# Performance work log

Measured on AMD Instinct MI355X. Metric: run time of the kernel, lower is better.

## Reference

```python
import jax, jax.numpy as jnp
import numpy as np

N = 50000
E = 400000
IN_FEATS = 256
HIDDEN = 64
HEADS = 8
CLASSES = 40
NEG_SLOPE = 0.2  # DGL GATConv default negative_slope


def setup_inputs() -> dict:
    key = jax.random.key(0)
    ks = jax.random.split(key, 12)
    features = jax.random.normal(ks[0], (N, IN_FEATS), dtype=jnp.float32)
    src = jax.random.randint(ks[1], (E,), 0, N, dtype=jnp.int32)
    dst = jax.random.randint(ks[2], (E,), 0, N, dtype=jnp.int32)
    s = 0.05
    # layer 0: in_feats -> HEADS*HIDDEN
    W1 = jax.random.normal(ks[3], (IN_FEATS, HEADS * HIDDEN), dtype=jnp.float32) * s
    al1 = jax.random.normal(ks[4], (HEADS, HIDDEN), dtype=jnp.float32) * s
    ar1 = jax.random.normal(ks[5], (HEADS, HIDDEN), dtype=jnp.float32) * s
    # layer 1: HEADS*HIDDEN -> HEADS*HIDDEN
    W2 = jax.random.normal(ks[6], (HEADS * HIDDEN, HEADS * HIDDEN), dtype=jnp.float32) * s
    al2 = jax.random.normal(ks[7], (HEADS, HIDDEN), dtype=jnp.float32) * s
    ar2 = jax.random.normal(ks[8], (HEADS, HIDDEN), dtype=jnp.float32) * s
    # layer 2: HEADS*HIDDEN -> 1*CLASSES
    W3 = jax.random.normal(ks[9], (HEADS * HIDDEN, CLASSES), dtype=jnp.float32) * s
    al3 = jax.random.normal(ks[10], (1, CLASSES), dtype=jnp.float32) * s
    ar3 = jax.random.normal(ks[11], (1, CLASSES), dtype=jnp.float32) * s
    return {"features": features, "src": src, "dst": dst,
            "W1": W1, "al1": al1, "ar1": ar1,
            "W2": W2, "al2": al2, "ar2": ar2,
            "W3": W3, "al3": al3, "ar3": ar3}


def gat_conv(h, W, al, ar, src, dst):
    """DGL GATConv (no bias, no residual, no activation, no dropout)."""
    H, D = al.shape
    feat = (h @ W).reshape(N, H, D)                      # [N,H,D]
    el = jnp.sum(feat * al[None], axis=-1)               # [N,H]
    er = jnp.sum(feat * ar[None], axis=-1)               # [N,H]
    e = jax.nn.leaky_relu(el[src] + er[dst], NEG_SLOPE)  # [E,H]
    # edge softmax over incoming edges of each dst node
    m = jax.ops.segment_max(e, dst, num_segments=N)      # [N,H]
    ex = jnp.exp(e - m[dst])                             # [E,H]
    denom = jax.ops.segment_sum(ex, dst, num_segments=N) # [N,H]
    alpha = ex / denom[dst]                              # [E,H]
    msg = alpha[:, :, None] * feat[src]                  # [E,H,D]
    out = jax.ops.segment_sum(msg, dst, num_segments=N)  # [N,H,D]
    return out.reshape(N, H * D)


def reference(features, src, dst, W1, al1, ar1, W2, al2, ar2, W3, al3, ar3):
    h = gat_conv(features, W1, al1, ar1, src, dst)  # [N, HEADS*HIDDEN]
    h = gat_conv(h, W2, al2, ar2, src, dst)         # [N, HEADS*HIDDEN]
    h = gat_conv(h, W3, al3, ar3, src, dst)         # [N, CLASSES]
    return h
```

## Files before the change

### kernel.cpp

```cpp
#include <hip/hip_runtime.h>
#include <hip/hip_bf16.h>

#define NN 50000
#define NE 400000
#define MPAD 50048

typedef __bf16 bf16x8_t __attribute__((ext_vector_type(8)));
typedef float f32x4_t __attribute__((ext_vector_type(4)));

__device__ __forceinline__ float bhi(unsigned int u) {
    union { unsigned int i; float f; } v; v.i = u & 0xffff0000u; return v.f;
}
__device__ __forceinline__ float blo(unsigned int u) {
    union { unsigned int i; float f; } v; v.i = u << 16; return v.f;
}

__global__ __launch_bounds__(256) void prep_kernel(
    const float* __restrict__ features, __hip_bfloat16* __restrict__ Abf,
    const int* __restrict__ dst, int* __restrict__ deg,
    const float* __restrict__ W1, __hip_bfloat16* __restrict__ W1t,
    const float* __restrict__ W2, __hip_bfloat16* __restrict__ W2t,
    const float* __restrict__ W3, __hip_bfloat16* __restrict__ W3t,
    const float* __restrict__ al1, const float* __restrict__ ar1,
    const float* __restrict__ al2, const float* __restrict__ ar2,
    __hip_bfloat16* __restrict__ walr1, __hip_bfloat16* __restrict__ walr2) {
    int stride = gridDim.x * blockDim.x;
    for (int i = blockIdx.x * blockDim.x + threadIdx.x; i < NN * 256; i += stride) {
        Abf[i] = __float2bfloat16(features[i]);
        if (i < NE) atomicAdd(&deg[dst[i]], 1);
        if (i < 512 * 256) {
            int n = i >> 8, k = i & 255;
            W1t[i] = __float2bfloat16(W1[k * 512 + n]);
        }
        if (i < 512 * 512) {
            int n = i >> 9, k = i & 511;
            W2t[i] = __float2bfloat16(W2[k * 512 + n]);
        }
        if (i < 48 * 512) {
            int n = i >> 9, k = i & 511;
            W3t[i] = __float2bfloat16((n < 40) ? W3[k * 40 + n] : 0.f);
        }
        if (i < 16 * 256) {
            int j = i >> 8, k = i & 255;
            const float* v = (j < 8) ? (al1 + j * 64) : (ar1 + (j - 8) * 64);
            float s = 0.f;
            for (int d = 0; d < 64; ++d) s += W1[(size_t)k * 512 + (j & 7) * 64 + d] * v[d];
            walr1[(k >> 5) * 512 + j * 32 + (k & 31)] = __float2bfloat16(s);
        }
        if (i < 16 * 512) {
            int j = i >> 9, k = i & 511;
            const float* v = (j < 8) ? (al2 + j * 64) : (ar2 + (j - 8) * 64);
            float s = 0.f;
            for (int d = 0; d < 64; ++d) s += W2[(size_t)k * 512 + (j & 7) * 64 + d] * v[d];
            walr2[(k >> 5) * 512 + j * 32 + (k & 31)] = __float2bfloat16(s);
        }
    }
}

__global__ void scan_kernel(const int* __restrict__ deg, int* __restrict__ off,
                            int* __restrict__ cur, int n) {
    __shared__ int wsum[16];
    __shared__ int carry_s;
    const int tid = threadIdx.x;
    const int lane = tid & 63, wid = tid >> 6;
    if (tid == 0) carry_s = 0;
    __syncthreads();
    for (int base = 0; base < n; base += 1024) {
        int i = base + tid;
        int v = (i < n) ? deg[i] : 0;
        int s = v;
        for (int o = 1; o < 64; o <<= 1) {
            int t = __shfl_up(s, o, 64);
            if (lane >= o) s += t;
        }
        if (lane == 63) wsum[wid] = s;
        __syncthreads();
        if (wid == 0) {
            int ws = (lane < 16) ? wsum[lane] : 0;
            for (int o = 1; o < 16; o <<= 1) {
                int t = __shfl_up(ws, o, 64);
                if (lane >= o) ws += t;
            }
            if (lane < 16) wsum[lane] = ws;
        }
        __syncthreads();
        int wpre = (wid == 0) ? 0 : wsum[wid - 1];
        int carry = carry_s;
        int excl = carry + wpre + s - v;
        if (i < n) { off[i] = excl; cur[i] = excl; }
        __syncthreads();
        if (tid == 1023) carry_s = carry + wsum[15];
    }
    __syncthreads();
    if (tid == 0) off[n] = carry_s;
}

__global__ void scatter_kernel(const int* __restrict__ src, const int* __restrict__ dst,
                               int* __restrict__ cur, int* __restrict__ csr_src) {
    int e = blockIdx.x * blockDim.x + threadIdx.x;
    if (e < NE) {
        int p = atomicAdd(&cur[dst[e]], 1);
        csr_src[p] = src[e];
    }
}

__device__ __forceinline__ void gld_lds16(const void* g, void* l) {
    __builtin_amdgcn_global_load_lds(
        (const __attribute__((address_space(1))) unsigned int*)g,
        (__attribute__((address_space(3))) unsigned int*)l, 16, 0, 0);
}

__global__ __launch_bounds__(256) void gemm_bt_fused(const __hip_bfloat16* __restrict__ A,
                                                     const __hip_bfloat16* __restrict__ Wt,
                                                     const __hip_bfloat16* __restrict__ walr,
                                                     __hip_bfloat16* __restrict__ C,
                                                     float* __restrict__ el,
                                                     float* __restrict__ er,
                                                     int K) {
    __shared__ __align__(16) char smem[16384];
    char* smemA = smem;
    char* smemB = smem + 8192;
    const int w = threadIdx.x >> 6;
    const int lane = threadIdx.x & 63;
    const int row0 = blockIdx.x * 128;
    const int col0 = blockIdx.y * 128;
    const int quad = lane >> 4, l15 = lane & 15;
    const int wm = (w >> 1) * 64, wn = (w & 1) * 64;
    const int c0 = w * 2;
    const int srow = lane >> 2;
    const int skel = (lane & 3) * 8;
    const bool my_e = (blockIdx.y == 0) && ((w & 1) == 0);

    f32x4_t acc[4][4] = {};
    f32x4_t acce[4] = {};
    for (int k0 = 0; k0 < K; k0 += 32) {
        __syncthreads();
        {
            const __hip_bfloat16* gA0 = A + (size_t)(row0 + c0 * 16 + srow) * K + k0 + skel;
            const __hip_bfloat16* gB0 = Wt + (size_t)(col0 + c0 * 16 + srow) * K + k0 + skel;
            gld_lds16(gA0, smemA + c0 * 1024);
            gld_lds16(gA0 + (size_t)16 * K, smemA + (c0 + 1) * 1024);
            gld_lds16(gB0, smemB + c0 * 1024);
            gld_lds16(gB0 + (size_t)16 * K, smemB + (c0 + 1) * 1024);
        }
        __syncthreads();
        bf16x8_t a[4], b[4];
#pragma unroll
        for (int mi = 0; mi < 4; mi++)
            a[mi] = *reinterpret_cast<const bf16x8_t*>(smemA + (wm + mi * 16 + l15) * 64 + quad * 16);
#pragma unroll
        for (int ni = 0; ni < 4; ni++)
            b[ni] = *reinterpret_cast<const bf16x8_t*>(smemB + (wn + ni * 16 + l15) * 64 + quad * 16);
#pragma unroll
        for (int mi = 0; mi < 4; mi++)
#pragma unroll
            for (int ni = 0; ni < 4; ni++)
                acc[mi][ni] = __builtin_amdgcn_mfma_f32_16x16x32_bf16(a[mi], b[ni], acc[mi][ni], 0, 0, 0);
        if (my_e) {
            bf16x8_t b5 = *reinterpret_cast<const bf16x8_t*>(
                walr + (k0 >> 5) * 512 + l15 * 32 + quad * 8);
#pragma unroll
            for (int mi = 0; mi < 4; mi++)
                acce[mi] = __builtin_amdgcn_mfma_f32_16x16x32_bf16(a[mi], b5, acce[mi], 0, 0, 0);
        }
    }
#pragma unroll
    for (int mi = 0; mi < 4; mi++) {
#pragma unroll
        for (int ni = 0; ni < 4; ni++) {
#pragma unroll
            for (int r = 0; r < 4; r++) {
                int row = row0 + wm + mi * 16 + quad * 4 + r;
                if (row < NN)
                    C[(size_t)row * 512 + col0 + wn + ni * 16 + l15] =
                        __float2bfloat16(acc[mi][ni][r]);
            }
        }
    }
    if (my_e) {
#pragma unroll
        for (int mi = 0; mi < 4; mi++) {
#pragma unroll
            for (int r = 0; r < 4; r++) {
                int row = row0 + wm + mi * 16 + quad * 4 + r;
                if (row < NN) {
                    float v = acce[mi][r];
                    if (l15 < 8) el[row * 8 + l15] = v;
                    else er[row * 8 + l15 - 8] = v;
                }
            }
        }
    }
}

#define W3_LDSROW 520
__global__ __launch_bounds__(256) void gemm3_mfma(const __hip_bfloat16* __restrict__ A,
                                                  const __hip_bfloat16* __restrict__ W3t,
                                                  const float* __restrict__ al,
                                                  const float* __restrict__ ar,
                                                  __hip_bfloat16* __restrict__ C,
                                                  float* __restrict__ el,
                                                  float* __restrict__ er) {
    __shared__ __align__(16) __hip_bfloat16 wlds[48 * W3_LDSROW];
    for (int c = threadIdx.x; c < 48 * 64; c += 256) {
        int n = c >> 6, koff = (c & 63) * 8;
        *reinterpret_cast<uint4*>(&wlds[n * W3_LDSROW + koff]) =
            *reinterpret_cast<const uint4*>(W3t + n * 512 + koff);
    }
    __syncthreads();
    const int w = threadIdx.x >> 6;
    const int lane = threadIdx.x & 63;
    const int quad = lane >> 4, l15 = lane & 15;
    const int row0 = blockIdx.x * 64 + w * 16;

    float alv[3], arv[3];
#pragma unroll
    for (int c = 0; c < 3; c++) {
        int col = c * 16 + l15;
        alv[c] = (col < 40) ? al[col] : 0.f;
        arv[c] = (col < 40) ? ar[col] : 0.f;
    }

    f32x4_t acc[3] = {};
    const __hip_bfloat16* arow = A + (size_t)(row0 + l15) * 512;
#pragma unroll 4
    for (int k0 = 0; k0 < 512; k0 += 32) {
        bf16x8_t a = *reinterpret_cast<const bf16x8_t*>(arow + k0 + quad * 8);
#pragma unroll
        for (int c = 0; c < 3; c++) {
            bf16x8_t b = *reinterpret_cast<const bf16x8_t*>(
                &wlds[(c * 16 + l15) * W3_LDSROW + k0 + quad * 8]);
            acc[c] = __builtin_amdgcn_mfma_f32_16x16x32_bf16(a, b, acc[c], 0, 0, 0);
        }
    }
#pragma unroll
    for (int r = 0; r < 4; r++) {
        int row = row0 + quad * 4 + r;
        bool rok = row < NN;
        float pl = 0.f, pr = 0.f;
#pragma unroll
        for (int c = 0; c < 3; c++) {
            float v = acc[c][r];
            if (rok) C[(size_t)row * 64 + c * 16 + l15] = __float2bfloat16(v);
            pl += v * alv[c];
            pr += v * arv[c];
        }
        if (rok) C[(size_t)row * 64 + 48 + l15] = __float2bfloat16(0.f);
        pl += __shfl_xor(pl, 1, 64); pr += __shfl_xor(pr, 1, 64);
        pl += __shfl_xor(pl, 2, 64); pr += __shfl_xor(pr, 2, 64);
        pl += __shfl_xor(pl, 4, 64); pr += __shfl_xor(pr, 4, 64);
        pl += __shfl_xor(pl, 8, 64); pr += __shfl_xor(pr, 8, 64);
        if (l15 == 0 && rok) { el[row] = pl; er[row] = pr; }
    }
}

__global__ __launch_bounds__(256) void agg8_kernel(const __hip_bfloat16* __restrict__ feat,
                                                   const float* __restrict__ el,
                                                   const float* __restrict__ er,
                                                   const int* __restrict__ off,
                                                   const int* __restrict__ csr,
                                                   __hip_bfloat16* __restrict__ out) {
    int n = (blockIdx.x * blockDim.x + threadIdx.x) >> 6;
    int lane = threadIdx.x & 63;
    if (n >= NN) return;
    const int h8 = lane & 7;
    const int es = lane >> 3;
    const int hd = lane >> 3;
    int rs = off[n], re = off[n + 1];
    float er_n = er[n * 8 + h8];

    float lsum = 0.f;
    float acc[8] = {};
    for (int base = rs; base < re; base += 16) {
        int e0 = base + es, e1 = base + 8 + es;
        bool v0 = e0 < re, v1 = e1 < re;
        int s0 = v0 ? csr[e0] : 0;
        int s1 = v1 ? csr[e1] : 0;
        float t0 = el[s0 * 8 + h8] + er_n;
        float t1 = el[s1 * 8 + h8] + er_n;
        float x0 = (t0 >= 0.f) ? t0 : 0.2f * t0;
        float x1 = (t1 >= 0.f) ? t1 : 0.2f * t1;
        float p0 = v0 ? __expf(x0) : 0.f;
        float p1 = v1 ? __expf(x1) : 0.f;
        lsum += p0 + p1;
        int cnt = min(16, re - base);
#pragma unroll
        for (int j = 0; j < 16; ++j) {
            if (j < cnt) {
                int srcl = (j & 7) * 8;
                int sj = __shfl((j < 8) ? s0 : s1, srcl, 64);
                float pj = __shfl((j < 8) ? p0 : p1, srcl + hd, 64);
                uint4 q = *reinterpret_cast<const uint4*>(feat + (size_t)sj * 512 + lane * 8);
                acc[0] += pj * blo(q.x); acc[1] += pj * bhi(q.x);
                acc[2] += pj * blo(q.y); acc[3] += pj * bhi(q.y);
                acc[4] += pj * blo(q.z); acc[5] += pj * bhi(q.z);
                acc[6] += pj * blo(q.w); acc[7] += pj * bhi(q.w);
            }
        }
    }
    lsum += __shfl_xor(lsum, 8, 64);
    lsum += __shfl_xor(lsum, 16, 64);
    lsum += __shfl_xor(lsum, 32, 64);
    float lh = __shfl(lsum, hd, 64);
    float inv = (lh > 0.f) ? 1.f / lh : 0.f;
    bf16x8_t o8;
#pragma unroll
    for (int d = 0; d < 8; ++d) o8[d] = (__bf16)(acc[d] * inv);
    *reinterpret_cast<bf16x8_t*>(out + (size_t)n * 512 + lane * 8) = o8;
}

__global__ __launch_bounds__(256) void agg3_kernel(const __hip_bfloat16* __restrict__ feat,
                                                   const float* __restrict__ el,
                                                   const float* __restrict__ er,
                                                   const int* __restrict__ off,
                                                   const int* __restrict__ csr,
                                                   float* __restrict__ out) {
    int n = (blockIdx.x * blockDim.x + threadIdx.x) >> 6;
    int lane = threadIdx.x & 63;
    if (n >= NN) return;
    const int es = lane >> 3;
    const int dc = lane & 7;
    int rs = off[n], re = off[n + 1];
    float er_n = er[n];

    float lsum = 0.f;
    float acc[8] = {};
    for (int base = rs; base < re; base += 16) {
        int e0 = base + es, e1 = base + 8 + es;
        bool v0 = e0 < re, v1 = e1 < re;
        int s0 = v0 ? csr[e0] : 0;
        int s1 = v1 ? csr[e1] : 0;
        float t0 = el[s0] + er_n;
        float t1 = el[s1] + er_n;
        float x0 = (t0 >= 0.f) ? t0 : 0.2f * t0;
        float x1 = (t1 >= 0.f) ? t1 : 0.2f * t1;
        float p0 = v0 ? __expf(x0) : 0.f;
        float p1 = v1 ? __expf(x1) : 0.f;
        lsum += p0 + p1;
        uint4 q0 = *reinterpret_cast<const uint4*>(feat + (size_t)s0 * 64 + dc * 8);
        uint4 q1 = *reinterpret_cast<const uint4*>(feat + (size_t)s1 * 64 + dc * 8);
        acc[0] += p0 * blo(q0.x) + p1 * blo(q1.x);
        acc[1] += p0 * bhi(q0.x) + p1 * bhi(q1.x);
        acc[2] += p0 * blo(q0.y) + p1 * blo(q1.y);
        acc[3] += p0 * bhi(q0.y) + p1 * bhi(q1.y);
        acc[4] += p0 * blo(q0.z) + p1 * blo(q1.z);
        acc[5] += p0 * bhi(q0.z) + p1 * bhi(q1.z);
        acc[6] += p0 * blo(q0.w) + p1 * blo(q1.w);
        acc[7] += p0 * bhi(q0.w) + p1 * bhi(q1.w);
    }
    lsum += __shfl_xor(lsum, 8, 64);
    lsum += __shfl_xor(lsum, 16, 64);
    lsum += __shfl_xor(lsum, 32, 64);
#pragma unroll
    for (int d = 0; d < 8; ++d) {
        acc[d] += __shfl_xor(acc[d], 8, 64);
        acc[d] += __shfl_xor(acc[d], 16, 64);
        acc[d] += __shfl_xor(acc[d], 32, 64);
    }
    float inv = (lsum > 0.f) ? 1.f / lsum : 0.f;
    if (es == 0 && dc < 5) {
        float4 o0 = make_float4(acc[0] * inv, acc[1] * inv, acc[2] * inv, acc[3] * inv);
        float4 o1 = make_float4(acc[4] * inv, acc[5] * inv, acc[6] * inv, acc[7] * inv);
        *reinterpret_cast<float4*>(out + (size_t)n * 40 + dc * 8) = o0;
        *reinterpret_cast<float4*>(out + (size_t)n * 40 + dc * 8 + 4) = o1;
    }
}

extern "C" void kernel_launch(void* const* d_in, const int* in_sizes, int n_in,
                              void* d_out, int out_size, void* d_ws, size_t ws_size,
                              hipStream_t stream) {
    const float* features = (const float*)d_in[0];
    const int* src = (const int*)d_in[1];
    const int* dst = (const int*)d_in[2];
    const float* W1 = (const float*)d_in[3];
    const float* al1 = (const float*)d_in[4];
    const float* ar1 = (const float*)d_in[5];
    const float* W2 = (const float*)d_in[6];
    const float* al2 = (const float*)d_in[7];
    const float* ar2 = (const float*)d_in[8];
    const float* W3 = (const float*)d_in[9];
    const float* al3 = (const float*)d_in[10];
    const float* ar3 = (const float*)d_in[11];

    char* ws = (char*)d_ws;
    size_t o = 0;
    auto carve = [&](size_t bytes) -> void* {
        o = (o + 255) & ~(size_t)255;
        void* p = ws + o;
        o += bytes;
        return p;
    };
    __hip_bfloat16* Abf1 = (__hip_bfloat16*)carve((size_t)MPAD * 256 * 2);
    __hip_bfloat16* Fbf = (__hip_bfloat16*)carve((size_t)MPAD * 512 * 2);
    __hip_bfloat16* Gbf = (__hip_bfloat16*)carve((size_t)MPAD * 512 * 2);
    __hip_bfloat16* W1t = (__hip_bfloat16*)carve((size_t)512 * 256 * 2);
    __hip_bfloat16* W2t = (__hip_bfloat16*)carve((size_t)512 * 512 * 2);
    __hip_bfloat16* W3t = (__hip_bfloat16*)carve((size_t)48 * 512 * 2);
    __hip_bfloat16* walr1 = (__hip_bfloat16*)carve((size_t)16 * 256 * 2);
    __hip_bfloat16* walr2 = (__hip_bfloat16*)carve((size_t)16 * 512 * 2);
    float* el = (float*)carve((size_t)NN * 8 * 4);
    float* er = (float*)carve((size_t)NN * 8 * 4);
    float* el3 = (float*)carve((size_t)NN * 4);
    float* er3 = (float*)carve((size_t)NN * 4);
    int* deg = (int*)carve((size_t)NN * 4);
    int* offp = (int*)carve((size_t)(NN + 1) * 4);
    int* cur = (int*)carve((size_t)NN * 4);
    int* csr = (int*)carve((size_t)NE * 4);

    hipMemsetAsync(deg, 0, (size_t)NN * 4, stream);
    prep_kernel<<<4096, 256, 0, stream>>>(features, Abf1, dst, deg, W1, W1t, W2, W2t, W3, W3t,
                                          al1, ar1, al2, ar2, walr1, walr2);
    scan_kernel<<<1, 1024, 0, stream>>>(deg, offp, cur, NN);
    scatter_kernel<<<(NE + 255) / 256, 256, 0, stream>>>(src, dst, cur, csr);

    const int gmm = MPAD / 128;
    const int aggblk = (NN + 3) / 4;
    gemm_bt_fused<<<dim3(gmm, 4), 256, 0, stream>>>(Abf1, W1t, walr1, Fbf, el, er, 256);
    agg8_kernel<<<aggblk, 256, 0, stream>>>(Fbf, el, er, offp, csr, Gbf);
    gemm_bt_fused<<<dim3(gmm, 4), 256, 0, stream>>>(Gbf, W2t, walr2, Fbf, el, er, 512);
    agg8_kernel<<<aggblk, 256, 0, stream>>>(Fbf, el, er, offp, csr, Gbf);
    gemm3_mfma<<<MPAD / 64, 256, 0, stream>>>(Gbf, W3t, al3, ar3, Fbf, el3, er3);
    agg3_kernel<<<aggblk, 256, 0, stream>>>(Fbf, el3, er3, offp, csr, (float*)d_out);
}
```

Baseline: 480.0 us.

## Fuse fp32-to-bf16 feature conversion into first GEMM and swizzle GEMM blocks per XCD

Removes the separate pass in prep_kernel that converted the 50000x256 fp32 feature matrix to bf16. A new gemm1_fused kernel instead loads fp32 rows directly, converts them in registers and writes the tile to LDS, which saves one full write and read of the intermediate. Both GEMMs now use a 1D grid with a block-index swizzle that places the four column tiles of a row block on the same XCD, aiming for better L2 reuse of A rows. The aggregation loop drops from 16 to 8 edges per iteration with a dynamic inner loop, trading unrolling and memory-level parallelism for less wasted work on low-degree nodes.

```diff
diff --git a/kernel.cpp b/kernel.cpp
--- a/kernel.cpp
+++ b/kernel.cpp
@@ -16,7 +16,6 @@
 }
 
 __global__ __launch_bounds__(256) void prep_kernel(
-    const float* __restrict__ features, __hip_bfloat16* __restrict__ Abf,
     const int* __restrict__ dst, int* __restrict__ deg,
     const float* __restrict__ W1, __hip_bfloat16* __restrict__ W1t,
     const float* __restrict__ W2, __hip_bfloat16* __restrict__ W2t,
@@ -25,9 +24,8 @@
     const float* __restrict__ al2, const float* __restrict__ ar2,
     __hip_bfloat16* __restrict__ walr1, __hip_bfloat16* __restrict__ walr2) {
     int stride = gridDim.x * blockDim.x;
-    for (int i = blockIdx.x * blockDim.x + threadIdx.x; i < NN * 256; i += stride) {
-        Abf[i] = __float2bfloat16(features[i]);
-        if (i < NE) atomicAdd(&deg[dst[i]], 1);
+    for (int i = blockIdx.x * blockDim.x + threadIdx.x; i < NE; i += stride) {
+        atomicAdd(&deg[dst[i]], 1);
         if (i < 512 * 256) {
             int n = i >> 8, k = i & 255;
             W1t[i] = __float2bfloat16(W1[k * 512 + n]);
@@ -104,10 +102,115 @@
     }
 }
 
+__device__ __forceinline__ bool swizzle(int g, int& row0, int& col0, int& ct) {
+    int xcd = g & 7;
+    ct = (g >> 3) & 3;
+    int row = (g >> 5) * 8 + xcd;
+    if (row >= 391) return false;
+    row0 = row * 128;
+    col0 = ct * 128;
+    return true;
+}
+
 __device__ __forceinline__ void gld_lds16(const void* g, void* l) {
     __builtin_amdgcn_global_load_lds(
         (const __attribute__((address_space(1))) unsigned int*)g,
         (__attribute__((address_space(3))) unsigned int*)l, 16, 0, 0);
+}
+
+__global__ __launch_bounds__(256) void gemm1_fused(const float* __restrict__ A,
+                                                   const __hip_bfloat16* __restrict__ Wt,
+                                                   const __hip_bfloat16* __restrict__ walr,
+                                                   __hip_bfloat16* __restrict__ C,
+                                                   float* __restrict__ el,
+                                                   float* __restrict__ er) {
+    const int K = 256;
+    __shared__ __align__(16) char smem[16384];
+    char* smemA = smem;
+    char* smemB = smem + 8192;
+    int row0, col0, ct;
+    if (!swizzle(blockIdx.x, row0, col0, ct)) return;
+    const int w = threadIdx.x >> 6;
+    const int lane = threadIdx.x & 63;
+    const int quad = lane >> 4, l15 = lane & 15;
+    const int wm = (w >> 1) * 64, wn = (w & 1) * 64;
+    const int c0 = w * 2;
+    const int srow = lane >> 2;
+    const int skel = (lane & 3) * 8;
+    const bool my_e = (ct == 0) && ((w & 1) == 0);
+
+    f32x4_t acc[4][4] = {};
+    f32x4_t acce[4] = {};
+    for (int k0 = 0; k0 < K; k0 += 32) {
+        __syncthreads();
+        {
+#pragma unroll
+            for (int cc = 0; cc < 2; ++cc) {
+                int row = row0 + (c0 + cc) * 16 + srow;
+                int rc = (row < NN) ? row : (NN - 1);
+                const float* p = A + (size_t)rc * K + k0 + skel;
+                float4 f0 = *reinterpret_cast<const float4*>(p);
+                float4 f1 = *reinterpret_cast<const float4*>(p + 4);
+                bf16x8_t h;
+                h[0] = (__bf16)f0.x; h[1] = (__bf16)f0.y;
+                h[2] = (__bf16)f0.z; h[3] = (__bf16)f0.w;
+                h[4] = (__bf16)f1.x; h[5] = (__bf16)f1.y;
+                h[6] = (__bf16)f1.z; h[7] = (__bf16)f1.w;
+                *reinterpret_cast<bf16x8_t*>(smemA + (c0 + cc) * 1024 + srow * 64 +
+                                             (lane & 3) * 16) = h;
+            }
+            const __hip_bfloat16* gB0 = Wt + (size_t)(col0 + c0 * 16 + srow) * K + k0 + skel;
+            gld_lds16(gB0, smemB + c0 * 1024);
+            gld_lds16(gB0 + (size_t)16 * K, smemB + (c0 + 1) * 1024);
+        }
+        __syncthreads();
+        bf16x8_t a[4], b[4];
+#pragma unroll
+        for (int mi = 0; mi < 4; mi++)
+            a[mi] = *reinterpret_cast<const bf16x8_t*>(smemA + (wm + mi * 16 + l15) * 64 + quad * 16);
+#pragma unroll
+        for (int ni = 0; ni < 4; ni++)
+            b[ni] = *reinterpret_cast<const bf16x8_t*>(smemB + (wn + ni * 16 + l15) * 64 + quad * 16);
+#pragma unroll
+        for (int mi = 0; mi < 4; mi++)
+#pragma unroll
+            for (int ni = 0; ni < 4; ni++)
+                acc[mi][ni] = __builtin_amdgcn_mfma_f32_16x16x32_bf16(a[mi], b[ni], acc[mi][ni], 0, 0, 0);
+        if (my_e) {
+            bf16x8_t b5 = *reinterpret_cast<const bf16x8_t*>(
+                walr + (k0 >> 5) * 512 + l15 * 32 + quad * 8);
+#pragma unroll
+            for (int mi = 0; mi < 4; mi++)
+                acce[mi] = __builtin_amdgcn_mfma_f32_16x16x32_bf16(a[mi], b5, acce[mi], 0, 0, 0);
+        }
+    }
+#pragma unroll
+    for (int mi = 0; mi < 4; mi++) {
+#pragma unroll
+        for (int ni = 0; ni < 4; ni++) {
+#pragma unroll
+            for (int r = 0; r < 4; r++) {
+                int row = row0 + wm + mi * 16 + quad * 4 + r;
+                if (row < NN)
+                    C[(size_t)row * 512 + col0 + wn + ni * 16 + l15] =
+                        __float2bfloat16(acc[mi][ni][r]);
+            }
+        }
+    }
+    if (my_e) {
+#pragma unroll
+        for (int mi = 0; mi < 4; mi++) {
+#pragma unroll
+            for (int r = 0; r < 4; r++) {
+                int row = row0 + wm + mi * 16 + quad * 4 + r;
+                if (row < NN) {
+                    float v = acce[mi][r];
+                    if (l15 < 8) el[row * 8 + l15] = v;
+                    else er[row * 8 + l15 - 8] = v;
+                }
+            }
+        }
+    }
 }
 
 __global__ __launch_bounds__(256) void gemm_bt_fused(const __hip_bfloat16* __restrict__ A,
@@ -115,21 +218,21 @@
                                                      const __hip_bfloat16* __restrict__ walr,
                                                      __hip_bfloat16* __restrict__ C,
                                                      float* __restrict__ el,
-                                                     float* __restrict__ er,
-                                                     int K) {
+                                                     float* __restrict__ er) {
+    const int K = 512;
     __shared__ __align__(16) char smem[16384];
     char* smemA = smem;
     char* smemB = smem + 8192;
+    int row0, col0, ct;
+    if (!swizzle(blockIdx.x, row0, col0, ct)) return;
     const int w = threadIdx.x >> 6;
     const int lane = threadIdx.x & 63;
-    const int row0 = blockIdx.x * 128;
-    const int col0 = blockIdx.y * 128;
     const int quad = lane >> 4, l15 = lane & 15;
     const int wm = (w >> 1) * 64, wn = (w & 1) * 64;
     const int c0 = w * 2;
     const int srow = lane >> 2;
     const int skel = (lane & 3) * 8;
-    const bool my_e = (blockIdx.y == 0) && ((w & 1) == 0);
+    const bool my_e = (ct == 0) && ((w & 1) == 0);
 
     f32x4_t acc[4][4] = {};
     f32x4_t acce[4] = {};
@@ -271,31 +374,23 @@
 
     float lsum = 0.f;
     float acc[8] = {};
-    for (int base = rs; base < re; base += 16) {
-        int e0 = base + es, e1 = base + 8 + es;
-        bool v0 = e0 < re, v1 = e1 < re;
-        int s0 = v0 ? csr[e0] : 0;
-        int s1 = v1 ? csr[e1] : 0;
-        float t0 = el[s0 * 8 + h8] + er_n;
-        float t1 = el[s1 * 8 + h8] + er_n;
-        float x0 = (t0 >= 0.f) ? t0 : 0.2f * t0;
-        float x1 = (t1 >= 0.f) ? t1 : 0.2f * t1;
-        float p0 = v0 ? __expf(x0) : 0.f;
-        float p1 = v1 ? __expf(x1) : 0.f;
-        lsum += p0 + p1;
-        int cnt = min(16, re - base);
-#pragma unroll
-        for (int j = 0; j < 16; ++j) {
-            if (j < cnt) {
-                int srcl = (j & 7) * 8;
-                int sj = __shfl((j < 8) ? s0 : s1, srcl, 64);
-                float pj = __shfl((j < 8) ? p0 : p1, srcl + hd, 64);
-                uint4 q = *reinterpret_cast<const uint4*>(feat + (size_t)sj * 512 + lane * 8);
-                acc[0] += pj * blo(q.x); acc[1] += pj * bhi(q.x);
-                acc[2] += pj * blo(q.y); acc[3] += pj * bhi(q.y);
-                acc[4] += pj * blo(q.z); acc[5] += pj * bhi(q.z);
-                acc[6] += pj * blo(q.w); acc[7] += pj * bhi(q.w);
-            }
+    for (int base = rs; base < re; base += 8) {
+        int e = base + es;
+        bool valid = e < re;
+        int s = valid ? csr[e] : 0;
+        float t = el[s * 8 + h8] + er_n;
+        float x = (t >= 0.f) ? t : 0.2f * t;
+        float p = valid ? __expf(x) : 0.f;
+        lsum += p;
+        int cnt = min(8, re - base);
+        for (int j = 0; j < cnt; ++j) {
+            int sj = __shfl(s, j * 8, 64);
+            float pj = __shfl(p, j * 8 + hd, 64);
+            uint4 q = *reinterpret_cast<const uint4*>(feat + (size_t)sj * 512 + lane * 8);
+            acc[0] += pj * blo(q.x); acc[1] += pj * bhi(q.x);
+            acc[2] += pj * blo(q.y); acc[3] += pj * bhi(q.y);
+            acc[4] += pj * blo(q.z); acc[5] += pj * bhi(q.z);
+            acc[6] += pj * blo(q.w); acc[7] += pj * bhi(q.w);
         }
     }
     lsum += __shfl_xor(lsum, 8, 64);
@@ -390,7 +485,6 @@
         o += bytes;
         return p;
     };
-    __hip_bfloat16* Abf1 = (__hip_bfloat16*)carve((size_t)MPAD * 256 * 2);
     __hip_bfloat16* Fbf = (__hip_bfloat16*)carve((size_t)MPAD * 512 * 2);
     __hip_bfloat16* Gbf = (__hip_bfloat16*)carve((size_t)MPAD * 512 * 2);
     __hip_bfloat16* W1t = (__hip_bfloat16*)carve((size_t)512 * 256 * 2);
@@ -408,16 +502,16 @@
     int* csr = (int*)carve((size_t)NE * 4);
 
     hipMemsetAsync(deg, 0, (size_t)NN * 4, stream);
-    prep_kernel<<<4096, 256, 0, stream>>>(features, Abf1, dst, deg, W1, W1t, W2, W2t, W3, W3t,
+    prep_kernel<<<1024, 256, 0, stream>>>(dst, deg, W1, W1t, W2, W2t, W3, W3t,
                                           al1, ar1, al2, ar2, walr1, walr2);
     scan_kernel<<<1, 1024, 0, stream>>>(deg, offp, cur, NN);
     scatter_kernel<<<(NE + 255) / 256, 256, 0, stream>>>(src, dst, cur, csr);
 
-    const int gmm = MPAD / 128;
+    const int gswz = 1568;
     const int aggblk = (NN + 3) / 4;
-    gemm_bt_fused<<<dim3(gmm, 4), 256, 0, stream>>>(Abf1, W1t, walr1, Fbf, el, er, 256);
+    gemm1_fused<<<gswz, 256, 0, stream>>>(features, W1t, walr1, Fbf, el, er);
     agg8_kernel<<<aggblk, 256, 0, stream>>>(Fbf, el, er, offp, csr, Gbf);
-    gemm_bt_fused<<<dim3(gmm, 4), 256, 0, stream>>>(Gbf, W2t, walr2, Fbf, el, er, 512);
+    gemm_bt_fused<<<gswz, 256, 0, stream>>>(Gbf, W2t, walr2, Fbf, el, er);
     agg8_kernel<<<aggblk, 256, 0, stream>>>(Fbf, el, er, offp, csr, Gbf);
     gemm3_mfma<<<MPAD / 64, 256, 0, stream>>>(Gbf, W3t, al3, ar3, Fbf, el3, er3);
     agg3_kernel<<<aggblk, 256, 0, stream>>>(Fbf, el3, er3, offp, csr, (float*)d_out);
```

Measured after the change: 485.8 us. About the same (+1.2%).
